# Kernel optimization log

Measured on AMD Instinct MI355X. Metric: run time of the kernel, lower is better.

Reference implementation:

```python
import jax, jax.numpy as jnp
import numpy as np

B, S, D, H = 2048, 71, 768, 4
DH = D // H          # 192 per-head dim
TEXT_LEN = 35
EPS = 1e-6


def setup_inputs() -> dict:
    key = jax.random.key(0)
    k1, k2, k3, k4, k5 = jax.random.split(key, 5)
    features = jax.random.normal(k1, (B, S, D), dtype=jnp.float32)
    attention_mask = jnp.ones((B, S), dtype=jnp.int32)  # unused by forward, kept for signature parity
    w_qkv = jax.random.normal(k2, (3 * D, D), dtype=jnp.float32) * 0.02
    b_qkv = jnp.zeros((3 * D,), dtype=jnp.float32)
    w_out = jax.random.normal(k3, (D, D), dtype=jnp.float32) * 0.02
    b_out = jnp.zeros((D,), dtype=jnp.float32)
    return {"features": features, "attention_mask": attention_mask,
            "w_qkv": w_qkv, "b_qkv": b_qkv, "w_out": w_out, "b_out": b_out}


def _linear_attention(x, w_qkv, b_qkv, w_out, b_out):
    # x: [B, S, D]
    qkv = jnp.einsum('bsd,ed->bse', x, w_qkv) + b_qkv          # [B, S, 3D]
    q, k, v = jnp.split(qkv, 3, axis=-1)
    q = q.reshape(B, S, H, DH)
    k = k.reshape(B, S, H, DH)
    v = v.reshape(B, S, H, DH)
    # kernel feature map phi(x) = elu(x) + 1 (Katharopoulos et al. linear attention)
    q = jax.nn.elu(q) + 1.0
    k = jax.nn.elu(k) + 1.0
    # non-causal linear attention: O(S * d^2) instead of O(S^2 * d)
    kv = jnp.einsum('bshd,bshe->bhde', k, v)                   # [B, H, DH, DH]
    z = jnp.sum(k, axis=1)                                     # [B, H, DH]
    num = jnp.einsum('bshd,bhde->bshe', q, kv)                 # [B, S, H, DH]
    den = jnp.einsum('bshd,bhd->bsh', q, z) + EPS              # [B, S, H]
    out = (num / den[..., None]).reshape(B, S, D)
    return jnp.einsum('bsd,ed->bse', out, w_out) + b_out


def reference(features, attention_mask, w_qkv, b_qkv, w_out, b_out):
    fused = _linear_attention(features, w_qkv, b_qkv, w_out, b_out)
    r_t = jnp.tanh(jnp.mean(fused[:, :TEXT_LEN], axis=1))       # [B, D]
    r_i = jnp.tanh(jnp.mean(fused[:, TEXT_LEN:], axis=1))       # [B, D]
    # cosine similarity along feature dim with torch's eps clamp (1e-8)
    nt = jnp.maximum(jnp.linalg.norm(r_t, axis=-1), 1e-8)
    ni = jnp.maximum(jnp.linalg.norm(r_i, axis=-1), 1e-8)
    return jnp.sum(r_t * r_i, axis=-1) / (nt * ni)              # [B]
```

## Files before the change

### kernel.cpp

```cpp
#include <hip/hip_runtime.h>
#include <hip/hip_bf16.h>

#define B_ 2048
#define S_ 71
#define SP 72
#define D_ 768
#define H_ 4
#define DH_ 192
#define TD2 1536
#define M_ (B_ * S_)
#define TEXT_ 35
#define NKT 12
#define NCH 852

typedef unsigned short u16;
typedef unsigned char u8;
typedef unsigned int u32;
typedef __attribute__((ext_vector_type(2))) float f32x2;
typedef __attribute__((ext_vector_type(4))) float f32x4;
typedef __attribute__((ext_vector_type(8))) short bf16x8;

__device__ __forceinline__ u16 f2bf(float f) {
  u32 u = __float_as_uint(f);
  u32 r = (u + 0x7FFFu + ((u >> 16) & 1u)) >> 16;
  return (u16)r;
}
__device__ __forceinline__ float bf2f(u16 x) {
  return __uint_as_float(((u32)x) << 16);
}
__device__ __forceinline__ u32 pk2bf(float lo, float hi) {
  __hip_bfloat162 h = __float22bfloat162_rn(float2{lo, hi});
  return *reinterpret_cast<u32*>(&h);
}

#if __has_builtin(__builtin_amdgcn_cvt_pk_fp8_f32) && __has_builtin(__builtin_amdgcn_cvt_pk_f32_fp8)
__device__ __forceinline__ u32 enc4fp8(float a, float b, float c, float d) {
  int w = 0;
  w = __builtin_amdgcn_cvt_pk_fp8_f32(a, b, w, false);
  w = __builtin_amdgcn_cvt_pk_fp8_f32(c, d, w, true);
  return (u32)w;
}
__device__ __forceinline__ void dec4f(u32 v, float* f) {
  f32x2 a = __builtin_amdgcn_cvt_pk_f32_fp8((int)v, false);
  f32x2 b = __builtin_amdgcn_cvt_pk_f32_fp8((int)v, true);
  f[0] = a.x; f[1] = a.y; f[2] = b.x; f[3] = b.y;
}
#else
__device__ __forceinline__ u8 f2fp8_1(float f) {
  f = fminf(f, 448.0f);
  u32 u = __float_as_uint(f);
  int e = (int)((u >> 23) & 0xFF) - 127;
  u32 m = u & 0x7FFFFF;
  u32 keep = m >> 20, rest = m & 0xFFFFF;
  u32 rb = (rest > 0x80000u) || (rest == 0x80000u && (keep & 1));
  u32 nrm = (((u32)(e + 7)) << 3) + keep + rb;
  u32 sub = (u32)__float2int_rn(f * 512.0f);
  u32 r = (e >= -6) ? nrm : ((e < -10) ? 0u : sub);
  return (u8)r;
}
__device__ __forceinline__ u32 enc4fp8(float a, float b, float c, float d) {
  return (u32)f2fp8_1(a) | ((u32)f2fp8_1(b) << 8) | ((u32)f2fp8_1(c) << 16) | ((u32)f2fp8_1(d) << 24);
}
__device__ __forceinline__ float fp82f(u32 v) {
  u32 e = (v >> 3) & 0xF, m = v & 7;
  float nrm = __uint_as_float(((e + 120) << 23) | (m << 20));
  return e ? nrm : (float)m * 0.001953125f;
}
__device__ __forceinline__ void dec4f(u32 v, float* f) {
  f[0] = fp82f(v & 0xFF); f[1] = fp82f((v >> 8) & 0xFF);
  f[2] = fp82f((v >> 16) & 0xFF); f[3] = fp82f(v >> 24);
}
#endif

typedef __attribute__((address_space(1))) const unsigned int GASU;
typedef __attribute__((address_space(3))) unsigned int LASU;
__device__ __forceinline__ void gload16(const void* g, void* l) {
  __builtin_amdgcn_global_load_lds((GASU*)g, (LASU*)l, 16, 0, 0);
}

#define PHASE_BAR() do { __builtin_amdgcn_s_barrier(); asm volatile("" ::: "memory"); } while (0)
#define LGKM0() do { asm volatile("s_waitcnt lgkmcnt(0)" ::: "memory"); __builtin_amdgcn_sched_barrier(0); } while (0)

__global__ __launch_bounds__(256) void k_cvt_bf16(const float* __restrict__ in,
                                                  u16* __restrict__ out, int n8) {
  int idx = blockIdx.x * 256 + threadIdx.x;
  if (idx >= n8) return;
  const float4* p = (const float4*)(in + (size_t)idx * 8);
  float4 a = p[0], b = p[1];
  uint4 o;
  o.x = pk2bf(a.x, a.y);
  o.y = pk2bf(a.z, a.w);
  o.z = pk2bf(b.x, b.y);
  o.w = pk2bf(b.z, b.w);
  *(uint4*)(out + (size_t)idx * 8) = o;
}

__global__ __launch_bounds__(512, 4) void k_gemm_qkv(
    const float* __restrict__ Afp,
    const u16* __restrict__ Bw,
    const float* __restrict__ bias,
    u8* __restrict__ C)
{
  __shared__ u16 sm[32768];
  int t = threadIdx.x;
  int lane = t & 63, wid = t >> 6;
  int wr = wid >> 2, wc = wid & 3;
  int lr = lane & 15;
  int g4 = lane >> 4;

  int swz = (blockIdx.x & 7) * 852 + (blockIdx.x >> 3);
  int bm = swz / 6, bn = swz % 6;
  const size_t arow0 = (size_t)bm * 128;
  const int bcol0 = bn * 256;

  const float* srcAf[2];
  int dA[2];
#pragma unroll
  for (int j = 0; j < 2; ++j) {
    int c = j * 512 + t;
    srcAf[j] = Afp + (arow0 + (c >> 3)) * 768 + ((c & 7) ^ ((c >> 3) & 7)) * 8;
    dA[j] = c * 8;
  }
  const u16* srcB[4];
  int dB[4];
#pragma unroll
  for (int j = 0; j < 4; ++j) {
    int c = j * 512 + t;
    srcB[j] = Bw + (size_t)(bcol0 + (c >> 3)) * 768 + ((c & 7) ^ ((c >> 3) & 7)) * 8;
    dB[j] = 16384 + c * 8;
  }

#define STAGE_B(ktu) do { \
  gload16(srcB[0] + (ktu), &sm[dB[0]]); \
  gload16(srcB[1] + (ktu), &sm[dB[1]]); \
  gload16(srcB[2] + (ktu), &sm[dB[2]]); \
  gload16(srcB[3] + (ktu), &sm[dB[3]]); \
} while (0)
#define LOADA(ktu) do { \
  fa0 = *(const float4*)(srcAf[0] + (ktu)); \
  fa1 = *(const float4*)(srcAf[0] + (ktu) + 4); \
  fa2 = *(const float4*)(srcAf[1] + (ktu)); \
  fa3 = *(const float4*)(srcAf[1] + (ktu) + 4); \
} while (0)
#define WRITEA(abuf) do { \
  uint4 o0; \
  o0.x = pk2bf(fa0.x, fa0.y); o0.y = pk2bf(fa0.z, fa0.w); \
  o0.z = pk2bf(fa1.x, fa1.y); o0.w = pk2bf(fa1.z, fa1.w); \
  *(uint4*)(&sm[(abuf) + dA[0]]) = o0; \
  uint4 o1; \
  o1.x = pk2bf(fa2.x, fa2.y); o1.y = pk2bf(fa2.z, fa2.w); \
  o1.z = pk2bf(fa3.x, fa3.y); o1.w = pk2bf(fa3.z, fa3.w); \
  *(uint4*)(&sm[(abuf) + dA[1]]) = o1; \
} while (0)

  int gx0 = g4 ^ (lr & 7);
  int aro = (wr * 64 + lr) * 64;
  int bro = 16384 + (wc * 64 + lr) * 64;

  f32x4 acc[4][4] = {};
  float4 fa0, fa1, fa2, fa3;

  LOADA(0);
  STAGE_B(0);
  asm volatile("s_waitcnt vmcnt(0)" ::: "memory");
  WRITEA(0);
  asm volatile("s_waitcnt lgkmcnt(0)" ::: "memory");
  PHASE_BAR();

  int curA = 0;
  for (int T = 0; T < NKT; ++T) {
    int nxtA = 8192 - curA;
    bool pf = (T < NKT - 1);
    int ktu = (T + 1) * 64;
    bf16x8 b0[4], a0[4];
#pragma unroll
    for (int ni = 0; ni < 4; ++ni) b0[ni] = *(const bf16x8*)(&sm[bro + ni * 1024 + gx0 * 8]);
#pragma unroll
    for (int mi = 0; mi < 4; ++mi) a0[mi] = *(const bf16x8*)(&sm[curA + aro + mi * 1024 + gx0 * 8]);
    __builtin_amdgcn_s_setprio(1);
#pragma unroll
    for (int mi = 0; mi < 4; ++mi)
#pragma unroll
      for (int ni = 0; ni < 4; ++ni)
        acc[mi][ni] = __builtin_amdgcn_mfma_f32_16x16x32_bf16(a0[mi], b0[ni], acc[mi][ni], 0, 0, 0);
    __builtin_amdgcn_s_setprio(0);
    int gx1 = gx0 ^ 4;
    bf16x8 b1[4];
#pragma unroll
    for (int ni = 0; ni < 4; ++ni) b1[ni] = *(const bf16x8*)(&sm[bro + ni * 1024 + gx1 * 8]);
    LGKM0();
    PHASE_BAR();
    if (pf) { STAGE_B(ktu); LOADA(ktu); }
    bf16x8 a1[4];
#pragma unroll
    for (int mi = 0; mi < 4; ++mi) a1[mi] = *(const bf16x8*)(&sm[curA + aro + mi * 1024 + gx1 * 8]);
    __builtin_amdgcn_s_setprio(1);
#pragma unroll
    for (int mi = 0; mi < 4; ++mi)
#pragma unroll
      for (int ni = 0; ni < 4; ++ni)
        acc[mi][ni] = __builtin_amdgcn_mfma_f32_16x16x32_bf16(a1[mi], b1[ni], acc[mi][ni], 0, 0, 0);
    __builtin_amdgcn_s_setprio(0);
    if (pf) {
      asm volatile("s_waitcnt vmcnt(0)" ::: "memory");
      WRITEA(nxtA);
      asm volatile("s_waitcnt lgkmcnt(0)" ::: "memory");
      PHASE_BAR();
    }
    curA = nxtA;
  }

#pragma unroll
  for (int mi = 0; mi < 4; ++mi) {
#pragma unroll
    for (int ni = 0; ni < 4; ++ni) {
      int col = bcol0 + wc * 64 + ni * 16 + lr;
      float bb = bias[col];
      float v[4];
#pragma unroll
      for (int i = 0; i < 4; ++i) {
        float x = acc[mi][ni][i] + bb;
        v[i] = (x > 0.0f) ? (x + 1.0f) : __expf(x);
      }
      u32 w = enc4fp8(v[0], v[1], v[2], v[3]);
      size_t r0 = arow0 + wr * 64 + mi * 16 + g4 * 4;
      C[(r0 + 0) * TD2 + col] = (u8)w;
      C[(r0 + 1) * TD2 + col] = (u8)(w >> 8);
      C[(r0 + 2) * TD2 + col] = (u8)(w >> 16);
      C[(r0 + 3) * TD2 + col] = (u8)(w >> 24);
    }
  }
#undef STAGE_B
#undef LOADA
#undef WRITEA
}

__global__ __launch_bounds__(256) void k_attn_qk(
    const u8* __restrict__ qk,
    float* __restrict__ AT,
    float* __restrict__ AI,
    float* __restrict__ sat)
{
  __shared__ u32 q8[S_ * 48];
  __shared__ u32 k8[S_ * 48];
  __shared__ float z[DH_], qt[DH_], qi[DH_];
  __shared__ float zqp[4][DH_];
  __shared__ float qip[4][DH_];
  __shared__ float wt[S_], wi[S_];
  __shared__ float at_l[S_ + 1], ai_l[S_ + 1];
  int t = threadIdx.x;
  int b = blockIdx.x >> 2, h = blockIdx.x & 3;
  size_t base = (size_t)b * S_ * TD2;
  int qoff = h * DH_, koff = 768 + h * DH_;
  int grp = t >> 4, gl = t & 15;
  int w = t >> 6, ln = t & 63;

#pragma unroll
  for (int j = 0; j < 4; ++j) {
    int c = j * 256 + t;
    int s = c / 12, cc = (c % 12) * 16;
    const u8* gq = qk + base + (size_t)s * TD2 + qoff + cc;
    const u8* gk = qk + base + (size_t)s * TD2 + koff + cc;
    char* dq = (char*)q8 + (size_t)(j * 256 + w * 64) * 16;
    char* dk = (char*)k8 + (size_t)(j * 256 + w * 64) * 16;
    if (c < NCH) {
      gload16(gq, dq);
      gload16(gk, dk);
    }
  }
  asm volatile("s_waitcnt vmcnt(0)" ::: "memory");
  __syncthreads();
  if (ln < 48) {
    int s0 = w * 18, s1 = (w == 3) ? S_ : (s0 + 18);
    float p[4] = {};
    for (int s = s0; s < s1; ++s) {
      float f[4];
      dec4f(k8[s * 48 + ln], f);
      p[0] += f[0]; p[1] += f[1]; p[2] += f[2]; p[3] += f[3];
    }
#pragma unroll
    for (int j = 0; j < 4; ++j) zqp[w][ln * 4 + j] = p[j];
  }
  __syncthreads();
  if (t < DH_) z[t] = (zqp[0][t] + zqp[1][t]) + (zqp[2][t] + zqp[3][t]);
  __syncthreads();
  for (int s = grp; s < S_; s += 16) {
    float f[12];
    int g0 = s * 48 + gl * 3;
    dec4f(q8[g0], f); dec4f(q8[g0 + 1], f + 4); dec4f(q8[g0 + 2], f + 8);
    float a = 0;
    int d0 = gl * 12;
#pragma unroll
    for (int i = 0; i < 12; ++i) a += f[i] * z[d0 + i];
#pragma unroll
    for (int o = 8; o >= 1; o >>= 1) a += __shfl_xor(a, o);
    if (gl == 0) {
      float den = a + 1e-6f;
      wt[s] = (s < TEXT_) ? 1.0f / (35.0f * den) : 0.0f;
      wi[s] = (s >= TEXT_) ? 1.0f / (36.0f * den) : 0.0f;
    }
  }
  __syncthreads();
  if (ln < 48) {
    int s0 = w * 18, s1 = (w == 3) ? S_ : (s0 + 18);
    float pt[4] = {}, pi[4] = {};
    for (int s = s0; s < s1; ++s) {
      float wts = wt[s], wis = wi[s];
      float f[4];
      dec4f(q8[s * 48 + ln], f);
#pragma unroll
      for (int j = 0; j < 4; ++j) { pt[j] += f[j] * wts; pi[j] += f[j] * wis; }
    }
#pragma unroll
    for (int j = 0; j < 4; ++j) { zqp[w][ln * 4 + j] = pt[j]; qip[w][ln * 4 + j] = pi[j]; }
  }
  __syncthreads();
  if (t < DH_) {
    qt[t] = (zqp[0][t] + zqp[1][t]) + (zqp[2][t] + zqp[3][t]);
    qi[t] = (qip[0][t] + qip[1][t]) + (qip[2][t] + qip[3][t]);
  }
  __syncthreads();
  size_t arow = ((size_t)b * 4 + h) * SP;
  for (int s = grp; s < S_; s += 16) {
    float f[12];
    int g0 = s * 48 + gl * 3;
    dec4f(k8[g0], f); dec4f(k8[g0 + 1], f + 4); dec4f(k8[g0 + 2], f + 8);
    float aT = 0, aI = 0;
    int d0 = gl * 12;
#pragma unroll
    for (int i = 0; i < 12; ++i) { aT += f[i] * qt[d0 + i]; aI += f[i] * qi[d0 + i]; }
#pragma unroll
    for (int o = 8; o >= 1; o >>= 1) { aT += __shfl_xor(aT, o); aI += __shfl_xor(aI, o); }
    if (gl == 0) {
      at_l[s] = aT; ai_l[s] = aI;
      AT[arow + s] = aT; AI[arow + s] = aI;
    }
  }
  __syncthreads();
  if (t < 64) {
    float vT = at_l[t] + ((t < 7) ? at_l[t + 64] : 0.0f);
    float vI = ai_l[t] + ((t < 7) ? ai_l[t + 64] : 0.0f);
#pragma unroll
    for (int o = 32; o >= 1; o >>= 1) { vT += __shfl_xor(vT, o); vI += __shfl_xor(vI, o); }
    if (t == 0) {
      sat[(size_t)b * 4 + h] = vT;
      sat[(size_t)(2048 + b) * 4 + h] = vI;
    }
  }
}

__global__ __launch_bounds__(192) void k_accy(
    const float* __restrict__ x,
    const float* __restrict__ AT,
    const float* __restrict__ AI,
    u16* __restrict__ Y)
{
  __shared__ float at_s[4][S_], ai_s[4][S_];
  int t = threadIdx.x, b = blockIdx.x;
  for (int i = t; i < 4 * S_; i += 192) {
    int h = i / S_, s = i % S_;
    at_s[h][s] = AT[((size_t)b * 4 + h) * SP + s];
    ai_s[h][s] = AI[((size_t)b * 4 + h) * SP + s];
  }
  __syncthreads();
  float4 yt[4] = {}, yi[4] = {};
  const float4* xb = (const float4*)(x + (size_t)b * S_ * 768);
  for (int s = 0; s < S_; ++s) {
    float4 xv = xb[s * 192 + t];
#pragma unroll
    for (int h = 0; h < 4; ++h) {
      float a = at_s[h][s], ai_ = ai_s[h][s];
      yt[h].x += a * xv.x; yt[h].y += a * xv.y; yt[h].z += a * xv.z; yt[h].w += a * xv.w;
      yi[h].x += ai_ * xv.x; yi[h].y += ai_ * xv.y; yi[h].z += ai_ * xv.z; yi[h].w += ai_ * xv.w;
    }
  }
  size_t rt = (size_t)b * 3072, ri = (size_t)(2048 + b) * 3072;
#pragma unroll
  for (int h = 0; h < 4; ++h) {
    uint2 ot, oi;
    ot.x = pk2bf(yt[h].x, yt[h].y); ot.y = pk2bf(yt[h].z, yt[h].w);
    oi.x = pk2bf(yi[h].x, yi[h].y); oi.y = pk2bf(yi[h].z, yi[h].w);
    *(uint2*)(&Y[rt + h * 768 + t * 4]) = ot;
    *(uint2*)(&Y[ri + h * 768 + t * 4]) = oi;
  }
}

__global__ __launch_bounds__(256, 4) void k_gemm_v(
    const u16* __restrict__ Yb,
    const u16* __restrict__ Wbf,
    const float* __restrict__ bqkv,
    const float* __restrict__ sat,
    u16* __restrict__ G)
{
  __shared__ u16 sm[24576];
  int t = threadIdx.x;
  int lane = t & 63, wid = t >> 6;
  int wr = wid >> 1, wc = wid & 1;
  int lr = lane & 15, g4 = lane >> 4;
  int bm = blockIdx.x / 12, nt = blockIdx.x % 12;
  int h = nt / 3, e0 = (nt % 3) * 64;
  const size_t arow0 = (size_t)bm * 128;

  const u16* srcA[4];
  int dA[4];
#pragma unroll
  for (int j = 0; j < 4; ++j) {
    int c = j * 256 + t;
    int row = c >> 3, kg = (c & 7) ^ (row & 7);
    srcA[j] = Yb + (arow0 + row) * 3072 + h * 768 + kg * 8;
    dA[j] = c * 8;
  }
  const u16* srcB[2];
  int dB[2];
#pragma unroll
  for (int j = 0; j < 2; ++j) {
    int c = j * 256 + t;
    int row = c >> 3, kg = (c & 7) ^ (row & 7);
    srcB[j] = Wbf + (size_t)(1536 + h * DH_ + e0 + row) * 768 + kg * 8;
    dB[j] = c * 8;
  }

#define VSTAGE(abuf, bbuf, ktu) do { \
  gload16(srcA[0] + (ktu), &sm[(abuf) + dA[0]]); \
  gload16(srcA[1] + (ktu), &sm[(abuf) + dA[1]]); \
  gload16(srcA[2] + (ktu), &sm[(abuf) + dA[2]]); \
  gload16(srcA[3] + (ktu), &sm[(abuf) + dA[3]]); \
  gload16(srcB[0] + (ktu), &sm[(bbuf) + dB[0]]); \
  gload16(srcB[1] + (ktu), &sm[(bbuf) + dB[1]]); \
} while (0)

  int gx0 = g4 ^ (lr & 7);
  int aro = (wr * 64 + lr) * 64;
  int bro = (wc * 32 + lr) * 64;

  f32x4 acc[4][2] = {};

  VSTAGE(0, 16384, 0);
  asm volatile("s_waitcnt vmcnt(0)" ::: "memory");
  PHASE_BAR();

  for (int T = 0; T < NKT; ++T) {
    int abuf = (T & 1) * 8192, bbuf = 16384 + (T & 1) * 4096;
    bool pf = (T < NKT - 1);
    if (pf) VSTAGE(8192 - abuf, 20480 - (T & 1) * 4096, (T + 1) * 64);
#pragma unroll
    for (int kk = 0; kk < 2; ++kk) {
      int gx = gx0 ^ (kk * 4);
      bf16x8 a[4], bfr[2];
#pragma unroll
      for (int mi = 0; mi < 4; ++mi) a[mi] = *(const bf16x8*)(&sm[abuf + aro + mi * 1024 + gx * 8]);
#pragma unroll
      for (int ni = 0; ni < 2; ++ni) bfr[ni] = *(const bf16x8*)(&sm[bbuf + bro + ni * 1024 + gx * 8]);
#pragma unroll
      for (int mi = 0; mi < 4; ++mi)
#pragma unroll
        for (int ni = 0; ni < 2; ++ni)
          acc[mi][ni] = __builtin_amdgcn_mfma_f32_16x16x32_bf16(a[mi], bfr[ni], acc[mi][ni], 0, 0, 0);
    }
    if (pf) {
      asm volatile("s_waitcnt vmcnt(0)" ::: "memory");
      PHASE_BAR();
    }
  }

#pragma unroll
  for (int mi = 0; mi < 4; ++mi) {
#pragma unroll
    for (int ni = 0; ni < 2; ++ni) {
      int e = e0 + wc * 32 + ni * 16 + lr;
      int gcol = h * DH_ + e;
      float bv = bqkv[1536 + gcol];
#pragma unroll
      for (int i = 0; i < 4; ++i) {
        size_t row = arow0 + wr * 64 + mi * 16 + g4 * 4 + i;
        G[row * 768 + gcol] = f2bf(acc[mi][ni][i] + sat[row * 4 + h] * bv);
      }
    }
  }
#undef VSTAGE
}

__global__ __launch_bounds__(512, 4) void k_gemm_head(
    const u16* __restrict__ Gb,
    const u16* __restrict__ Wo,
    const float* __restrict__ bout,
    u16* __restrict__ F)
{
  __shared__ u16 sm[32768];
  int t = threadIdx.x;
  int lane = t & 63, wid = t >> 6;
  int wr = wid >> 2, wc = wid & 3;
  int lr = lane & 15;
  int g4 = lane >> 4;

  int bm = blockIdx.x / 3, bn = blockIdx.x % 3;
  const size_t arow0 = (size_t)bm * 128;
  const int bcol0 = bn * 256;

  const u16* srcA[2];
  int dA[2];
#pragma unroll
  for (int j = 0; j < 2; ++j) {
    int c = j * 512 + t;
    srcA[j] = Gb + (arow0 + (c >> 3)) * 768 + ((c & 7) ^ ((c >> 3) & 7)) * 8;
    dA[j] = c * 8;
  }
  const u16* srcB[4];
  int dB[4];
#pragma unroll
  for (int j = 0; j < 4; ++j) {
    int c = j * 512 + t;
    srcB[j] = Wo + (size_t)(bcol0 + (c >> 3)) * 768 + ((c & 7) ^ ((c >> 3) & 7)) * 8;
    dB[j] = 16384 + c * 8;
  }

#define STAGE_A2(abuf, ktu) do { \
  gload16(srcA[0] + (ktu), &sm[(abuf) + dA[0]]); \
  gload16(srcA[1] + (ktu), &sm[(abuf) + dA[1]]); \
} while (0)
#define STAGE_B2(ktu) do { \
  gload16(srcB[0] + (ktu), &sm[dB[0]]); \
  gload16(srcB[1] + (ktu), &sm[dB[1]]); \
  gload16(srcB[2] + (ktu), &sm[dB[2]]); \
  gload16(srcB[3] + (ktu), &sm[dB[3]]); \
} while (0)

  int gx0 = g4 ^ (lr & 7);
  int aro = (wr * 64 + lr) * 64;
  int bro = 16384 + (wc * 64 + lr) * 64;

  f32x4 acc[4][4] = {};

  STAGE_A2(0, 0); STAGE_B2(0);
  asm volatile("s_waitcnt vmcnt(0)" ::: "memory");
  PHASE_BAR();

  int curA = 0;
  for (int T = 0; T < NKT; ++T) {
    int nxtA = 8192 - curA;
    bool pf = (T < NKT - 1);
    int ktu = (T + 1) * 64;
    bf16x8 bfr[4][2];
#pragma unroll
    for (int ni = 0; ni < 4; ++ni) {
      bfr[ni][0] = *(const bf16x8*)(&sm[bro + ni * 1024 + gx0 * 8]);
      bfr[ni][1] = *(const bf16x8*)(&sm[bro + ni * 1024 + (gx0 ^ 4) * 8]);
    }
    LGKM0();
    PHASE_BAR();
    if (pf) { STAGE_B2(ktu); STAGE_A2(nxtA, ktu); }
    __builtin_amdgcn_s_setprio(1);
#pragma unroll
    for (int kk = 0; kk < 2; ++kk) {
      int gx = gx0 ^ (kk * 4);
      bf16x8 afr[4];
#pragma unroll
      for (int mi = 0; mi < 4; ++mi)
        afr[mi] = *(const bf16x8*)(&sm[curA + aro + mi * 1024 + gx * 8]);
#pragma unroll
      for (int mi = 0; mi < 4; ++mi)
#pragma unroll
        for (int ni = 0; ni < 4; ++ni)
          acc[mi][ni] = __builtin_amdgcn_mfma_f32_16x16x32_bf16(afr[mi], bfr[ni][kk], acc[mi][ni], 0, 0, 0);
    }
    __builtin_amdgcn_s_setprio(0);
    if (pf) {
      asm volatile("s_waitcnt vmcnt(0)" ::: "memory");
      PHASE_BAR();
    }
    curA = nxtA;
  }

#pragma unroll
  for (int mi = 0; mi < 4; ++mi) {
#pragma unroll
    for (int ni = 0; ni < 4; ++ni) {
      int col = bcol0 + wc * 64 + ni * 16 + lr;
      float bb = bout[col];
#pragma unroll
      for (int i = 0; i < 4; ++i) {
        size_t row = arow0 + wr * 64 + mi * 16 + g4 * 4 + i;
        F[row * 768 + col] = f2bf(tanhf(acc[mi][ni][i] + bb));
      }
    }
  }
#undef STAGE_A2
#undef STAGE_B2
}

#define GC 4
__global__ __launch_bounds__(256) void k_cos(
    const u16* __restrict__ F,
    float* __restrict__ out)
{
  __shared__ float red[3][4];
  int t = threadIdx.x, b0 = blockIdx.x * GC;
  int lane = t & 63, wid = t >> 6;
  for (int g = 0; g < GC; ++g) {
    int b = b0 + g;
    float st = 0, si = 0, sd = 0;
#pragma unroll
    for (int j = 0; j < 3; ++j) {
      int c = t + j * 256;
      float rt = bf2f(F[(size_t)b * 768 + c]);
      float ri = bf2f(F[(size_t)(2048 + b) * 768 + c]);
      st += rt * rt; si += ri * ri; sd += rt * ri;
    }
#pragma unroll
    for (int off = 32; off >= 1; off >>= 1) {
      st += __shfl_down(st, off);
      si += __shfl_down(si, off);
      sd += __shfl_down(sd, off);
    }
    __syncthreads();
    if (lane == 0) { red[0][wid] = st; red[1][wid] = si; red[2][wid] = sd; }
    __syncthreads();
    if (t == 0) {
      float S1 = red[0][0] + red[0][1] + red[0][2] + red[0][3];
      float S2 = red[1][0] + red[1][1] + red[1][2] + red[1][3];
      float S3 = red[2][0] + red[2][1] + red[2][2] + red[2][3];
      out[b] = S3 / (fmaxf(sqrtf(S1), 1e-8f) * fmaxf(sqrtf(S2), 1e-8f));
    }
  }
}

extern "C" void kernel_launch(void* const* d_in, const int* in_sizes, int n_in,
                              void* d_out, int out_size, void* d_ws, size_t ws_size,
                              hipStream_t stream) {
  const float* features = (const float*)d_in[0];
  const float* w_qkv = (const float*)d_in[2];
  const float* b_qkv = (const float*)d_in[3];
  const float* w_out = (const float*)d_in[4];
  const float* b_out = (const float*)d_in[5];
  float* out = (float*)d_out;

  char* ws = (char*)d_ws;
  size_t off = 0;
  auto alloc = [&](size_t bytes) {
    void* p = ws + off;
    off += (bytes + 255) & ~(size_t)255;
    return p;
  };
  u8*  QK   = (u8*)alloc((size_t)M_ * TD2);
  u16* Wbf  = (u16*)alloc((size_t)2304 * D_ * 2);
  u16* Wobf = (u16*)alloc((size_t)D_ * D_ * 2);
  u16* Yv   = (u16*)alloc((size_t)4096 * 3072 * 2);
  float* AT = (float*)alloc((size_t)B_ * 4 * SP * 4);
  float* AI = (float*)alloc((size_t)B_ * 4 * SP * 4);
  float* sat = (float*)alloc((size_t)4096 * 4 * 4);
  u16* G    = (u16*)alloc((size_t)4096 * D_ * 2);
  u16* F    = (u16*)alloc((size_t)4096 * D_ * 2);
  (void)ws_size;

  hipLaunchKernelGGL(k_cvt_bf16, dim3((2304 * D_ / 8 + 255) / 256), dim3(256), 0, stream,
                     w_qkv, Wbf, 2304 * D_ / 8);
  hipLaunchKernelGGL(k_cvt_bf16, dim3((D_ * D_ / 8 + 255) / 256), dim3(256), 0, stream,
                     w_out, Wobf, D_ * D_ / 8);

  hipLaunchKernelGGL(k_gemm_qkv, dim3(6 * 1136), dim3(512), 0, stream,
                     features, Wbf, b_qkv, QK);
  hipLaunchKernelGGL(k_attn_qk, dim3(B_ * H_), dim3(256), 0, stream, QK, AT, AI, sat);
  hipLaunchKernelGGL(k_accy, dim3(B_), dim3(192), 0, stream, features, AT, AI, Yv);
  hipLaunchKernelGGL(k_gemm_v, dim3(32 * 12), dim3(256), 0, stream,
                     Yv, Wbf, b_qkv, sat, G);
  hipLaunchKernelGGL(k_gemm_head, dim3(32 * 3), dim3(512), 0, stream,
                     G, Wobf, b_out, F);
  hipLaunchKernelGGL(k_cos, dim3(B_ / GC), dim3(256), 0, stream, F, out);
}
```

Baseline: 636.0 us.

## Run QK projection GEMM in FP8 with scaled FP8 weights and doubled K-tile

The Q/K projection GEMM now converts activations to FP8 on the fly and uses FP8 weights pre-scaled by 64. It runs MFMA fp8 instructions with a 128-wide K tile, so there are half as many main-loop iterations, and the epilogue undoes the scale. The V weights get their own bf16 buffer, and the fallback software FP8 encoder/decoder gains sign handling. This is meant to halve LDS and global bytes per K step and to use the higher FP8 MFMA rate. The cost is reduced precision in the Q/K features, which could hurt accuracy.

```diff
diff --git a/kernel.cpp b/kernel.cpp
--- a/kernel.cpp
+++ b/kernel.cpp
@@ -11,11 +11,13 @@
 #define M_ (B_ * S_)
 #define TEXT_ 35
 #define NKT 12
+#define NK8 6
 #define NCH 852
 
 typedef unsigned short u16;
 typedef unsigned char u8;
 typedef unsigned int u32;
+typedef long long i64;
 typedef __attribute__((ext_vector_type(2))) float f32x2;
 typedef __attribute__((ext_vector_type(4))) float f32x4;
 typedef __attribute__((ext_vector_type(8))) short bf16x8;
@@ -47,6 +49,8 @@
 }
 #else
 __device__ __forceinline__ u8 f2fp8_1(float f) {
+  float sgn = (f < 0.f) ? -1.f : 1.f;
+  f = fabsf(f);
   f = fminf(f, 448.0f);
   u32 u = __float_as_uint(f);
   int e = (int)((u >> 23) & 0xFF) - 127;
@@ -56,19 +60,20 @@
   u32 nrm = (((u32)(e + 7)) << 3) + keep + rb;
   u32 sub = (u32)__float2int_rn(f * 512.0f);
   u32 r = (e >= -6) ? nrm : ((e < -10) ? 0u : sub);
-  return (u8)r;
+  return (u8)(r | (sgn < 0.f ? 0x80u : 0u));
 }
 __device__ __forceinline__ u32 enc4fp8(float a, float b, float c, float d) {
   return (u32)f2fp8_1(a) | ((u32)f2fp8_1(b) << 8) | ((u32)f2fp8_1(c) << 16) | ((u32)f2fp8_1(d) << 24);
 }
-__device__ __forceinline__ float fp82f(u32 v) {
-  u32 e = (v >> 3) & 0xF, m = v & 7;
+__device__ __forceinline__ float fp82f1(u32 v) {
+  u32 s = v >> 7, e = (v >> 3) & 0xF, m = v & 7;
   float nrm = __uint_as_float(((e + 120) << 23) | (m << 20));
-  return e ? nrm : (float)m * 0.001953125f;
+  float r = e ? nrm : (float)m * 0.001953125f;
+  return s ? -r : r;
 }
 __device__ __forceinline__ void dec4f(u32 v, float* f) {
-  f[0] = fp82f(v & 0xFF); f[1] = fp82f((v >> 8) & 0xFF);
-  f[2] = fp82f((v >> 16) & 0xFF); f[3] = fp82f(v >> 24);
+  f[0] = fp82f1(v & 0xFF); f[1] = fp82f1((v >> 8) & 0xFF);
+  f[2] = fp82f1((v >> 16) & 0xFF); f[3] = fp82f1(v >> 24);
 }
 #endif
 
@@ -95,13 +100,27 @@
   *(uint4*)(out + (size_t)idx * 8) = o;
 }
 
+__global__ __launch_bounds__(256) void k_cvt_w8(const float* __restrict__ in,
+                                                u8* __restrict__ out, int n16) {
+  int idx = blockIdx.x * 256 + threadIdx.x;
+  if (idx >= n16) return;
+  const float4* p = (const float4*)(in + (size_t)idx * 16);
+  float4 a = p[0], b = p[1], c = p[2], d = p[3];
+  uint4 o;
+  o.x = enc4fp8(a.x * 64.f, a.y * 64.f, a.z * 64.f, a.w * 64.f);
+  o.y = enc4fp8(b.x * 64.f, b.y * 64.f, b.z * 64.f, b.w * 64.f);
+  o.z = enc4fp8(c.x * 64.f, c.y * 64.f, c.z * 64.f, c.w * 64.f);
+  o.w = enc4fp8(d.x * 64.f, d.y * 64.f, d.z * 64.f, d.w * 64.f);
+  *(uint4*)(out + (size_t)idx * 16) = o;
+}
+
 __global__ __launch_bounds__(512, 4) void k_gemm_qkv(
     const float* __restrict__ Afp,
-    const u16* __restrict__ Bw,
+    const u8* __restrict__ Wf8,
     const float* __restrict__ bias,
     u8* __restrict__ C)
 {
-  __shared__ u16 sm[32768];
+  __shared__ u8 sm8[65536];
   int t = threadIdx.x;
   int lane = t & 63, wid = t >> 6;
   int wr = wid >> 2, wc = wid & 3;
@@ -118,92 +137,103 @@
 #pragma unroll
   for (int j = 0; j < 2; ++j) {
     int c = j * 512 + t;
-    srcAf[j] = Afp + (arow0 + (c >> 3)) * 768 + ((c & 7) ^ ((c >> 3) & 7)) * 8;
-    dA[j] = c * 8;
-  }
-  const u16* srcB[4];
+    int row = c >> 3, cc = c & 7;
+    srcAf[j] = Afp + (arow0 + row) * 768 + ((cc ^ (row & 7)) * 16);
+    dA[j] = c * 16;
+  }
+  const u8* srcB[4];
   int dB[4];
 #pragma unroll
   for (int j = 0; j < 4; ++j) {
     int c = j * 512 + t;
-    srcB[j] = Bw + (size_t)(bcol0 + (c >> 3)) * 768 + ((c & 7) ^ ((c >> 3) & 7)) * 8;
-    dB[j] = 16384 + c * 8;
+    int row = c >> 3, cc = c & 7;
+    srcB[j] = Wf8 + (size_t)(bcol0 + row) * 768 + ((cc ^ (row & 7)) * 16);
+    dB[j] = 32768 + c * 16;
   }
 
 #define STAGE_B(ktu) do { \
-  gload16(srcB[0] + (ktu), &sm[dB[0]]); \
-  gload16(srcB[1] + (ktu), &sm[dB[1]]); \
-  gload16(srcB[2] + (ktu), &sm[dB[2]]); \
-  gload16(srcB[3] + (ktu), &sm[dB[3]]); \
+  gload16(srcB[0] + (ktu), &sm8[dB[0]]); \
+  gload16(srcB[1] + (ktu), &sm8[dB[1]]); \
+  gload16(srcB[2] + (ktu), &sm8[dB[2]]); \
+  gload16(srcB[3] + (ktu), &sm8[dB[3]]); \
 } while (0)
-#define LOADA(ktu) do { \
-  fa0 = *(const float4*)(srcAf[0] + (ktu)); \
-  fa1 = *(const float4*)(srcAf[0] + (ktu) + 4); \
-  fa2 = *(const float4*)(srcAf[1] + (ktu)); \
-  fa3 = *(const float4*)(srcAf[1] + (ktu) + 4); \
+#define LOADA(j, ktu) do { \
+  const float4* p_ = (const float4*)(srcAf[j] + (ktu)); \
+  fa0 = p_[0]; fa1 = p_[1]; fa2 = p_[2]; fa3 = p_[3]; \
 } while (0)
-#define WRITEA(abuf) do { \
-  uint4 o0; \
-  o0.x = pk2bf(fa0.x, fa0.y); o0.y = pk2bf(fa0.z, fa0.w); \
-  o0.z = pk2bf(fa1.x, fa1.y); o0.w = pk2bf(fa1.z, fa1.w); \
-  *(uint4*)(&sm[(abuf) + dA[0]]) = o0; \
-  uint4 o1; \
-  o1.x = pk2bf(fa2.x, fa2.y); o1.y = pk2bf(fa2.z, fa2.w); \
-  o1.z = pk2bf(fa3.x, fa3.y); o1.w = pk2bf(fa3.z, fa3.w); \
-  *(uint4*)(&sm[(abuf) + dA[1]]) = o1; \
+#define WRITEA(j, abuf) do { \
+  uint4 o_; \
+  o_.x = enc4fp8(fa0.x, fa0.y, fa0.z, fa0.w); \
+  o_.y = enc4fp8(fa1.x, fa1.y, fa1.z, fa1.w); \
+  o_.z = enc4fp8(fa2.x, fa2.y, fa2.z, fa2.w); \
+  o_.w = enc4fp8(fa3.x, fa3.y, fa3.z, fa3.w); \
+  *(uint4*)(&sm8[(abuf) + dA[j]]) = o_; \
 } while (0)
 
-  int gx0 = g4 ^ (lr & 7);
-  int aro = (wr * 64 + lr) * 64;
-  int bro = 16384 + (wc * 64 + lr) * 64;
+  int offk[4];
+#pragma unroll
+  for (int kk = 0; kk < 4; ++kk)
+    offk[kk] = (((kk * 2 + (g4 >> 1)) ^ (lr & 7)) * 16) + (g4 & 1) * 8;
+  int aro = (wr * 64 + lr) * 128;
+  int bro = 32768 + (wc * 64 + lr) * 128;
 
   f32x4 acc[4][4] = {};
   float4 fa0, fa1, fa2, fa3;
 
-  LOADA(0);
+  LOADA(0, 0);
   STAGE_B(0);
+  asm volatile("s_waitcnt vmcnt(16)" ::: "memory");
+  WRITEA(0, 0);
+  LOADA(1, 0);
   asm volatile("s_waitcnt vmcnt(0)" ::: "memory");
-  WRITEA(0);
+  WRITEA(1, 0);
   asm volatile("s_waitcnt lgkmcnt(0)" ::: "memory");
   PHASE_BAR();
 
   int curA = 0;
-  for (int T = 0; T < NKT; ++T) {
-    int nxtA = 8192 - curA;
-    bool pf = (T < NKT - 1);
-    int ktu = (T + 1) * 64;
-    bf16x8 b0[4], a0[4];
-#pragma unroll
-    for (int ni = 0; ni < 4; ++ni) b0[ni] = *(const bf16x8*)(&sm[bro + ni * 1024 + gx0 * 8]);
-#pragma unroll
-    for (int mi = 0; mi < 4; ++mi) a0[mi] = *(const bf16x8*)(&sm[curA + aro + mi * 1024 + gx0 * 8]);
-    __builtin_amdgcn_s_setprio(1);
-#pragma unroll
-    for (int mi = 0; mi < 4; ++mi)
-#pragma unroll
-      for (int ni = 0; ni < 4; ++ni)
-        acc[mi][ni] = __builtin_amdgcn_mfma_f32_16x16x32_bf16(a0[mi], b0[ni], acc[mi][ni], 0, 0, 0);
-    __builtin_amdgcn_s_setprio(0);
-    int gx1 = gx0 ^ 4;
-    bf16x8 b1[4];
-#pragma unroll
-    for (int ni = 0; ni < 4; ++ni) b1[ni] = *(const bf16x8*)(&sm[bro + ni * 1024 + gx1 * 8]);
+  for (int T = 0; T < NK8; ++T) {
+    int nxtA = 16384 - curA;
+    bool pf = (T < NK8 - 1);
+    int ktu = (T + 1) * 128;
+    i64 b3[4];
+#pragma unroll
+    for (int kk = 0; kk < 3; ++kk) {
+      i64 bfr[4], afr[4];
+#pragma unroll
+      for (int ni = 0; ni < 4; ++ni) bfr[ni] = *(const i64*)(&sm8[bro + ni * 2048 + offk[kk]]);
+#pragma unroll
+      for (int mi = 0; mi < 4; ++mi) afr[mi] = *(const i64*)(&sm8[curA + aro + mi * 2048 + offk[kk]]);
+      __builtin_amdgcn_s_setprio(1);
+#pragma unroll
+      for (int mi = 0; mi < 4; ++mi)
+#pragma unroll
+        for (int ni = 0; ni < 4; ++ni)
+          acc[mi][ni] = __builtin_amdgcn_mfma_f32_16x16x32_fp8_fp8((long)afr[mi], (long)bfr[ni], acc[mi][ni], 0, 0, 0);
+      __builtin_amdgcn_s_setprio(0);
+    }
+#pragma unroll
+    for (int ni = 0; ni < 4; ++ni) b3[ni] = *(const i64*)(&sm8[bro + ni * 2048 + offk[3]]);
     LGKM0();
     PHASE_BAR();
-    if (pf) { STAGE_B(ktu); LOADA(ktu); }
-    bf16x8 a1[4];
-#pragma unroll
-    for (int mi = 0; mi < 4; ++mi) a1[mi] = *(const bf16x8*)(&sm[curA + aro + mi * 1024 + gx1 * 8]);
+    if (pf) { LOADA(0, ktu); STAGE_B(ktu); }
+    i64 a3[4];
+#pragma unroll
+    for (int mi = 0; mi < 4; ++mi) a3[mi] = *(const i64*)(&sm8[curA + aro + mi * 2048 + offk[3]]);
+    if (pf) {
+      asm volatile("s_waitcnt vmcnt(16)" ::: "memory");
+      WRITEA(0, nxtA);
+      LOADA(1, ktu);
+    }
     __builtin_amdgcn_s_setprio(1);
 #pragma unroll
     for (int mi = 0; mi < 4; ++mi)
 #pragma unroll
       for (int ni = 0; ni < 4; ++ni)
-        acc[mi][ni] = __builtin_amdgcn_mfma_f32_16x16x32_bf16(a1[mi], b1[ni], acc[mi][ni], 0, 0, 0);
+        acc[mi][ni] = __builtin_amdgcn_mfma_f32_16x16x32_fp8_fp8((long)a3[mi], (long)b3[ni], acc[mi][ni], 0, 0, 0);
     __builtin_amdgcn_s_setprio(0);
     if (pf) {
       asm volatile("s_waitcnt vmcnt(0)" ::: "memory");
-      WRITEA(nxtA);
+      WRITEA(1, nxtA);
       asm volatile("s_waitcnt lgkmcnt(0)" ::: "memory");
       PHASE_BAR();
     }
@@ -219,7 +249,7 @@
       float v[4];
 #pragma unroll
       for (int i = 0; i < 4; ++i) {
-        float x = acc[mi][ni][i] + bb;
+        float x = acc[mi][ni][i] * 0.015625f + bb;
         v[i] = (x > 0.0f) ? (x + 1.0f) : __expf(x);
       }
       u32 w = enc4fp8(v[0], v[1], v[2], v[3]);
@@ -387,7 +417,7 @@
 
 __global__ __launch_bounds__(256, 4) void k_gemm_v(
     const u16* __restrict__ Yb,
-    const u16* __restrict__ Wbf,
+    const u16* __restrict__ Wvbf,
     const float* __restrict__ bqkv,
     const float* __restrict__ sat,
     u16* __restrict__ G)
@@ -416,7 +446,7 @@
   for (int j = 0; j < 2; ++j) {
     int c = j * 256 + t;
     int row = c >> 3, kg = (c & 7) ^ (row & 7);
-    srcB[j] = Wbf + (size_t)(1536 + h * DH_ + e0 + row) * 768 + kg * 8;
+    srcB[j] = Wvbf + (size_t)(h * DH_ + e0 + row) * 768 + kg * 8;
     dB[j] = c * 8;
   }
 
@@ -642,7 +672,8 @@
     return p;
   };
   u8*  QK   = (u8*)alloc((size_t)M_ * TD2);
-  u16* Wbf  = (u16*)alloc((size_t)2304 * D_ * 2);
+  u8*  Wf8  = (u8*)alloc((size_t)TD2 * D_);
+  u16* Wvbf = (u16*)alloc((size_t)D_ * D_ * 2);
   u16* Wobf = (u16*)alloc((size_t)D_ * D_ * 2);
   u16* Yv   = (u16*)alloc((size_t)4096 * 3072 * 2);
   float* AT = (float*)alloc((size_t)B_ * 4 * SP * 4);
@@ -652,17 +683,19 @@
   u16* F    = (u16*)alloc((size_t)4096 * D_ * 2);
   (void)ws_size;
 
-  hipLaunchKernelGGL(k_cvt_bf16, dim3((2304 * D_ / 8 + 255) / 256), dim3(256), 0, stream,
-                     w_qkv, Wbf, 2304 * D_ / 8);
+  hipLaunchKernelGGL(k_cvt_w8, dim3((TD2 * D_ / 16 + 255) / 256), dim3(256), 0, stream,
+                     w_qkv, Wf8, TD2 * D_ / 16);
+  hipLaunchKernelGGL(k_cvt_bf16, dim3((D_ * D_ / 8 + 255) / 256), dim3(256), 0, stream,
+                     w_qkv + (size_t)TD2 * D_, Wvbf, D_ * D_ / 8);
   hipLaunchKernelGGL(k_cvt_bf16, dim3((D_ * D_ / 8 + 255) / 256), dim3(256), 0, stream,
                      w_out, Wobf, D_ * D_ / 8);
 
   hipLaunchKernelGGL(k_gemm_qkv, dim3(6 * 1136), dim3(512), 0, stream,
-                     features, Wbf, b_qkv, QK);
+                     features, Wf8, b_qkv, QK);
   hipLaunchKernelGGL(k_attn_qk, dim3(B_ * H_), dim3(256), 0, stream, QK, AT, AI, sat);
   hipLaunchKernelGGL(k_accy, dim3(B_), dim3(192), 0, stream, features, AT, AI, Yv);
   hipLaunchKernelGGL(k_gemm_v, dim3(32 * 12), dim3(256), 0, stream,
-                     Yv, Wbf, b_qkv, sat, G);
+                     Yv, Wvbf, b_qkv, sat, G);
   hipLaunchKernelGGL(k_gemm_head, dim3(32 * 3), dim3(512), 0, stream,
                      G, Wobf, b_out, F);
   hipLaunchKernelGGL(k_cos, dim3(B_ / GC), dim3(256), 0, stream, F, out);
```

Result: faster. 612.1 us (-3.8%).
